# Kernel tuning notes

Hardware: AMD Instinct MI355X
Metric: run time of the kernel (lower is better)

The kernel has to match this reference:

```python
import jax, jax.numpy as jnp
import numpy as np

EPS = 1e-5


def setup_inputs() -> dict:
    key = jax.random.key(0)
    ks = jax.random.split(key, 7)
    B, T, H = 4, 4096, 1024
    x = jax.random.normal(ks[0], (B, T, H), dtype=jnp.float32)
    gamma = jnp.ones((H,), dtype=jnp.float32)
    beta = jnp.zeros((H,), dtype=jnp.float32)
    s = 1.0 / np.sqrt(H)
    Wg = jax.random.uniform(ks[1], (H, H), minval=-s, maxval=s, dtype=jnp.float32)
    bg = jax.random.uniform(ks[2], (H,), minval=-s, maxval=s, dtype=jnp.float32)
    Wc = jax.random.uniform(ks[3], (H, H), minval=-s, maxval=s, dtype=jnp.float32)
    bc = jax.random.uniform(ks[4], (H,), minval=-s, maxval=s, dtype=jnp.float32)
    return {"x": x, "gamma": gamma, "beta": beta, "Wg": Wg, "bg": bg, "Wc": Wc, "bc": bc}


def reference(x, gamma, beta, Wg, bg, Wc, bc):
    # x: [B, T, H]
    mu = jnp.mean(x, axis=-1, keepdims=True)
    var = jnp.mean((x - mu) ** 2, axis=-1, keepdims=True)
    normed = (x - mu) * jax.lax.rsqrt(var + EPS) * gamma + beta
    z = jax.nn.sigmoid(jnp.einsum('bth,oh->bto', normed, Wg) + bg)  # gate
    c = jnp.einsum('bth,oh->bto', normed, Wc) + bc                  # candidate
    B, T, H = x.shape

    def step(h, zc):
        z_t, c_t = zc  # each [B, H]
        h = (1.0 - z_t) * h + z_t * c_t
        return h, h

    h0 = jnp.zeros((B, H), dtype=x.dtype)
    # scan over time: move T to leading axis
    _, hs = jax.lax.scan(step, h0, (jnp.swapaxes(z, 0, 1), jnp.swapaxes(c, 0, 1)))
    return jnp.swapaxes(hs, 0, 1) + x  # residual
```

## Files before the change

kernel.cpp:

```cpp
#include <hip/hip_runtime.h>
#include <stdint.h>


#define B_    4
#define T_    4096
#define H_    1024
#define BT_   (B_*T_)
#define EPSV  1e-5f
#define CHK   32
#define CL    (T_/CHK)

typedef float  f32x4  __attribute__((ext_vector_type(4)));
typedef __bf16 bf16x8 __attribute__((ext_vector_type(8)));
typedef unsigned short u16;

__device__ __forceinline__ u16 f2bf(float f) {
  uint32_t u = __builtin_bit_cast(uint32_t, f);
  u += 0x7fffu + ((u >> 16) & 1u);
  return (u16)(u >> 16);
}
__device__ __forceinline__ float bf2f(u16 u) {
  uint32_t v = ((uint32_t)u) << 16;
  return __builtin_bit_cast(float, v);
}

__global__ __launch_bounds__(256) void ln_kernel(
    const float* __restrict__ x, const float* __restrict__ gamma,
    const float* __restrict__ beta, u16* __restrict__ normed) {
  const int row = blockIdx.x;
  const int tid = threadIdx.x;
  const float4 v = reinterpret_cast<const float4*>(x + (size_t)row * H_)[tid];
  float s = v.x + v.y + v.z + v.w;
  float q = v.x*v.x + v.y*v.y + v.z*v.z + v.w*v.w;
  #pragma unroll
  for (int off = 32; off > 0; off >>= 1) {
    s += __shfl_down(s, off);
    q += __shfl_down(q, off);
  }
  __shared__ float ls[8], lq[8];
  const int wid = tid >> 6, lane = tid & 63;
  if (lane == 0) { ls[wid] = s; lq[wid] = q; }
  __syncthreads();
  if (tid == 0) {
    ls[4] = ls[0] + ls[1] + ls[2] + ls[3];
    lq[4] = lq[0] + lq[1] + lq[2] + lq[3];
  }
  __syncthreads();
  const float mean = ls[4] * (1.0f / H_);
  const float var  = lq[4] * (1.0f / H_) - mean * mean;
  const float rstd = rsqrtf(var + EPSV);
  const float4 g  = reinterpret_cast<const float4*>(gamma)[tid];
  const float4 bb = reinterpret_cast<const float4*>(beta)[tid];
  uint2 o;
  o.x = (uint32_t)f2bf((v.x - mean) * rstd * g.x + bb.x)
      | ((uint32_t)f2bf((v.y - mean) * rstd * g.y + bb.y) << 16);
  o.y = (uint32_t)f2bf((v.z - mean) * rstd * g.z + bb.z)
      | ((uint32_t)f2bf((v.w - mean) * rstd * g.w + bb.w) << 16);
  reinterpret_cast<uint2*>(normed + (size_t)row * H_)[tid] = o;
}

__global__ __launch_bounds__(256) void pack_kernel(
    const float* __restrict__ Wg, const float* __restrict__ Wc,
    u16* __restrict__ wpack) {
  const int idx4 = (blockIdx.x * 256 + threadIdx.x) * 4;
  const int n = idx4 >> 10;
  const int k = idx4 & 1023;
  const float* src = (n < 1024) ? (Wg + (size_t)n * 1024 + k)
                                : (Wc + (size_t)(n - 1024) * 1024 + k);
  const float4 v = *reinterpret_cast<const float4*>(src);
  uint2 o;
  o.x = (uint32_t)f2bf(v.x) | ((uint32_t)f2bf(v.y) << 16);
  o.y = (uint32_t)f2bf(v.z) | ((uint32_t)f2bf(v.w) << 16);
  *reinterpret_cast<uint2*>(wpack + idx4) = o;
}

__global__ __launch_bounds__(256) void gemm_kernel(
    const u16* __restrict__ A, const u16* __restrict__ Bw,
    const float* __restrict__ bg, const float* __restrict__ bc,
    u16* __restrict__ zbuf, u16* __restrict__ cbuf) {
  __shared__ u16 As[128 * 32];
  __shared__ u16 Bs[128 * 32];
  const int bid = blockIdx.x;
  const int nb  = (bid & 7) * 256 + (bid >> 3);
  const int mt  = nb >> 4, nt = nb & 15;
  const int tid = threadIdx.x;
  const int wid = tid >> 6, lane = tid & 63;
  const int wr = wid >> 1, wcq = wid & 1;

  f32x4 acc[4][4] = {};

  const int c0 = tid, c1 = tid + 256;
  const u16* a0 = A  + (size_t)(mt * 128 + (c0 >> 2)) * 1024 + (c0 & 3) * 8;
  const u16* a1 = A  + (size_t)(mt * 128 + (c1 >> 2)) * 1024 + (c1 & 3) * 8;
  const u16* b0 = Bw + (size_t)(nt * 128 + (c0 >> 2)) * 1024 + (c0 & 3) * 8;
  const u16* b1 = Bw + (size_t)(nt * 128 + (c1 >> 2)) * 1024 + (c1 & 3) * 8;

  const int frow = lane & 15;
  const int kb   = (lane >> 4) * 8;

  for (int ks = 0; ks < 32; ++ks) {
    const int kk = ks * 32;
    __builtin_amdgcn_global_load_lds(
        (const __attribute__((address_space(1))) void*)(a0 + kk),
        (__attribute__((address_space(3))) void*)&As[c0 * 8], 16, 0, 0);
    __builtin_amdgcn_global_load_lds(
        (const __attribute__((address_space(1))) void*)(a1 + kk),
        (__attribute__((address_space(3))) void*)&As[c1 * 8], 16, 0, 0);
    __builtin_amdgcn_global_load_lds(
        (const __attribute__((address_space(1))) void*)(b0 + kk),
        (__attribute__((address_space(3))) void*)&Bs[c0 * 8], 16, 0, 0);
    __builtin_amdgcn_global_load_lds(
        (const __attribute__((address_space(1))) void*)(b1 + kk),
        (__attribute__((address_space(3))) void*)&Bs[c1 * 8], 16, 0, 0);
    __syncthreads();

    bf16x8 af[4], bfr[4];
    #pragma unroll
    for (int m = 0; m < 4; ++m)
      af[m] = *reinterpret_cast<const bf16x8*>(&As[(wr * 64 + m * 16 + frow) * 32 + kb]);
    #pragma unroll
    for (int n = 0; n < 4; ++n)
      bfr[n] = *reinterpret_cast<const bf16x8*>(&Bs[(wcq * 64 + n * 16 + frow) * 32 + kb]);
    #pragma unroll
    for (int m = 0; m < 4; ++m)
      #pragma unroll
      for (int n = 0; n < 4; ++n)
        acc[m][n] = __builtin_amdgcn_mfma_f32_16x16x32_bf16(af[m], bfr[n], acc[m][n], 0, 0, 0);
    __syncthreads();
  }

  const int r0  = (lane >> 4) * 4;
  const int col16 = lane & 15;
  const bool isz = (nt < 8);
  #pragma unroll
  for (int m = 0; m < 4; ++m) {
    #pragma unroll
    for (int n = 0; n < 4; ++n) {
      const int col = nt * 128 + wcq * 64 + n * 16 + col16;
      #pragma unroll
      for (int r = 0; r < 4; ++r) {
        const int row = mt * 128 + wr * 64 + m * 16 + r0 + r;
        float v = acc[m][n][r];
        if (isz) {
          v += bg[col];
          v = 1.0f / (1.0f + __expf(-v));
          zbuf[(size_t)row * 1024 + col] = f2bf(v);
        } else {
          const int cc = col - 1024;
          v += bc[cc];
          cbuf[(size_t)row * 1024 + cc] = f2bf(v);
        }
      }
    }
  }
}

__global__ __launch_bounds__(256) void scan1_kernel(
    const u16* __restrict__ zbuf, const u16* __restrict__ cbuf,
    float* __restrict__ Achk, float* __restrict__ Uchk) {
  const int bid   = blockIdx.x;
  const int o     = (bid & 3) * 256 + threadIdx.x;
  const int chunk = (bid >> 2) & 31;
  const int b     = bid >> 7;
  const size_t base = ((size_t)(b * T_ + chunk * CL)) * H_ + o;
  float A = 1.0f, u = 0.0f;
  #pragma unroll 8
  for (int t = 0; t < CL; ++t) {
    const float z = bf2f(zbuf[base + (size_t)t * H_]);
    const float c = bf2f(cbuf[base + (size_t)t * H_]);
    const float a = 1.0f - z;
    A *= a;
    u = a * u + z * c;
  }
  const int idx = (b * CHK + chunk) * H_ + o;
  Achk[idx] = A;
  Uchk[idx] = u;
}

__global__ __launch_bounds__(256) void scan2_kernel(
    const float* __restrict__ Achk, const float* __restrict__ Uchk,
    float* __restrict__ Hin) {
  const int bid = blockIdx.x;
  const int o   = (bid & 3) * 256 + threadIdx.x;
  const int b   = bid >> 2;
  float h = 0.0f;
  for (int j = 0; j < CHK; ++j) {
    const int idx = (b * CHK + j) * H_ + o;
    Hin[idx] = h;
    h = Achk[idx] * h + Uchk[idx];
  }
}

__global__ __launch_bounds__(256) void scan3_kernel(
    const u16* __restrict__ zbuf, const u16* __restrict__ cbuf,
    const float* __restrict__ Hin, const float* __restrict__ x,
    float* __restrict__ out) {
  const int bid   = blockIdx.x;
  const int o     = (bid & 3) * 256 + threadIdx.x;
  const int chunk = (bid >> 2) & 31;
  const int b     = bid >> 7;
  float h = Hin[(b * CHK + chunk) * H_ + o];
  const size_t base = ((size_t)(b * T_ + chunk * CL)) * H_ + o;
  #pragma unroll 4
  for (int t = 0; t < CL; ++t) {
    const size_t idx = base + (size_t)t * H_;
    const float z = bf2f(zbuf[idx]);
    const float c = bf2f(cbuf[idx]);
    h = (1.0f - z) * h + z * c;
    out[idx] = h + x[idx];
  }
}

extern "C" void kernel_launch(void* const* d_in, const int* in_sizes, int n_in,
                              void* d_out, int out_size, void* d_ws, size_t ws_size,
                              hipStream_t stream) {
  const float* x     = (const float*)d_in[0];
  const float* gamma = (const float*)d_in[1];
  const float* beta  = (const float*)d_in[2];
  const float* Wg    = (const float*)d_in[3];
  const float* bg    = (const float*)d_in[4];
  const float* Wc    = (const float*)d_in[5];
  const float* bc    = (const float*)d_in[6];
  float* out = (float*)d_out;

  char* ws = (char*)d_ws;
  u16*   normed = (u16*)(ws);
  u16*   wpack  = (u16*)(ws + 33554432ull);
  u16*   zbuf   = (u16*)(ws + 37748736ull);
  u16*   cbuf   = (u16*)(ws + 71303168ull);
  float* Achk   = (float*)(ws + 104857600ull);
  float* Uchk   = (float*)(ws + 105381888ull);
  float* Hin    = (float*)(ws + 105906176ull);

  ln_kernel  <<<BT_,  256, 0, stream>>>(x, gamma, beta, normed);
  pack_kernel<<<2048, 256, 0, stream>>>(Wg, Wc, wpack);
  gemm_kernel<<<2048, 256, 0, stream>>>(normed, wpack, bg, bc, zbuf, cbuf);
  scan1_kernel<<<512, 256, 0, stream>>>(zbuf, cbuf, Achk, Uchk);
  scan2_kernel<<<16,  256, 0, stream>>>(Achk, Uchk, Hin);
  scan3_kernel<<<512, 256, 0, stream>>>(zbuf, cbuf, Hin, x, out);
}
```

Baseline: 287.0 us.

## Double-buffer GEMM LDS, vectorize scans, warp-per-row layernorm, finer scan chunks

Several changes land together. The GEMM now double-buffers its LDS tiles so the next K-slice is fetched while the current one is computed. LayerNorm handles one row per wavefront with xor shuffles, which removes the shared-memory reduction and both barriers. The scan kernels move to 128 chunks with each thread handling four columns through vectorized bf16 and float loads, and the chunk-state buffers now reuse the normed region of the workspace. The gain in parallelism and load width is paid for with more LDS per GEMM block and a longer serial pass in scan2.

```diff
diff --git a/kernel.cpp b/kernel.cpp
--- a/kernel.cpp
+++ b/kernel.cpp
@@ -7,7 +7,7 @@
 #define H_    1024
 #define BT_   (B_*T_)
 #define EPSV  1e-5f
-#define CHK   32
+#define CHK   128
 #define CL    (T_/CHK)
 
 typedef float  f32x4  __attribute__((ext_vector_type(4)));
@@ -19,44 +19,51 @@
   u += 0x7fffu + ((u >> 16) & 1u);
   return (u16)(u >> 16);
 }
-__device__ __forceinline__ float bf2f(u16 u) {
-  uint32_t v = ((uint32_t)u) << 16;
+__device__ __forceinline__ float bf2f(uint32_t u) {
+  uint32_t v = (u & 0xffffu) << 16;
   return __builtin_bit_cast(float, v);
+}
+__device__ __forceinline__ void bf4(uint2 p, float* f) {
+  f[0] = bf2f(p.x); f[1] = bf2f(p.x >> 16);
+  f[2] = bf2f(p.y); f[3] = bf2f(p.y >> 16);
 }
 
 __global__ __launch_bounds__(256) void ln_kernel(
     const float* __restrict__ x, const float* __restrict__ gamma,
     const float* __restrict__ beta, u16* __restrict__ normed) {
-  const int row = blockIdx.x;
-  const int tid = threadIdx.x;
-  const float4 v = reinterpret_cast<const float4*>(x + (size_t)row * H_)[tid];
-  float s = v.x + v.y + v.z + v.w;
-  float q = v.x*v.x + v.y*v.y + v.z*v.z + v.w*v.w;
-  #pragma unroll
-  for (int off = 32; off > 0; off >>= 1) {
-    s += __shfl_down(s, off);
-    q += __shfl_down(q, off);
-  }
-  __shared__ float ls[8], lq[8];
-  const int wid = tid >> 6, lane = tid & 63;
-  if (lane == 0) { ls[wid] = s; lq[wid] = q; }
-  __syncthreads();
-  if (tid == 0) {
-    ls[4] = ls[0] + ls[1] + ls[2] + ls[3];
-    lq[4] = lq[0] + lq[1] + lq[2] + lq[3];
-  }
-  __syncthreads();
-  const float mean = ls[4] * (1.0f / H_);
-  const float var  = lq[4] * (1.0f / H_) - mean * mean;
+  const int wid  = threadIdx.x >> 6, lane = threadIdx.x & 63;
+  const int row  = blockIdx.x * 4 + wid;
+  const float4* xr = reinterpret_cast<const float4*>(x + (size_t)row * H_);
+  float4 v[4];
+  float s = 0.0f, q = 0.0f;
+  #pragma unroll
+  for (int seg = 0; seg < 4; ++seg) {
+    v[seg] = xr[seg * 64 + lane];
+    s += v[seg].x + v[seg].y + v[seg].z + v[seg].w;
+    q += v[seg].x*v[seg].x + v[seg].y*v[seg].y + v[seg].z*v[seg].z + v[seg].w*v[seg].w;
+  }
+  #pragma unroll
+  for (int off = 1; off < 64; off <<= 1) {
+    s += __shfl_xor(s, off);
+    q += __shfl_xor(q, off);
+  }
+  const float mean = s * (1.0f / H_);
+  const float var  = q * (1.0f / H_) - mean * mean;
   const float rstd = rsqrtf(var + EPSV);
-  const float4 g  = reinterpret_cast<const float4*>(gamma)[tid];
-  const float4 bb = reinterpret_cast<const float4*>(beta)[tid];
-  uint2 o;
-  o.x = (uint32_t)f2bf((v.x - mean) * rstd * g.x + bb.x)
-      | ((uint32_t)f2bf((v.y - mean) * rstd * g.y + bb.y) << 16);
-  o.y = (uint32_t)f2bf((v.z - mean) * rstd * g.z + bb.z)
-      | ((uint32_t)f2bf((v.w - mean) * rstd * g.w + bb.w) << 16);
-  reinterpret_cast<uint2*>(normed + (size_t)row * H_)[tid] = o;
+  const float4* g4 = reinterpret_cast<const float4*>(gamma);
+  const float4* b4 = reinterpret_cast<const float4*>(beta);
+  uint2* o2 = reinterpret_cast<uint2*>(normed + (size_t)row * H_);
+  #pragma unroll
+  for (int seg = 0; seg < 4; ++seg) {
+    const float4 g = g4[seg * 64 + lane];
+    const float4 b = b4[seg * 64 + lane];
+    uint2 o;
+    o.x = (uint32_t)f2bf((v[seg].x - mean) * rstd * g.x + b.x)
+        | ((uint32_t)f2bf((v[seg].y - mean) * rstd * g.y + b.y) << 16);
+    o.y = (uint32_t)f2bf((v[seg].z - mean) * rstd * g.z + b.z)
+        | ((uint32_t)f2bf((v[seg].w - mean) * rstd * g.w + b.w) << 16);
+    o2[seg * 64 + lane] = o;
+  }
 }
 
 __global__ __launch_bounds__(256) void pack_kernel(
@@ -78,8 +85,8 @@
     const u16* __restrict__ A, const u16* __restrict__ Bw,
     const float* __restrict__ bg, const float* __restrict__ bc,
     u16* __restrict__ zbuf, u16* __restrict__ cbuf) {
-  __shared__ u16 As[128 * 32];
-  __shared__ u16 Bs[128 * 32];
+  __shared__ u16 As[2][128 * 32];
+  __shared__ u16 Bs[2][128 * 32];
   const int bid = blockIdx.x;
   const int nb  = (bid & 7) * 256 + (bid >> 3);
   const int mt  = nb >> 4, nt = nb & 15;
@@ -98,36 +105,46 @@
   const int frow = lane & 15;
   const int kb   = (lane >> 4) * 8;
 
-  for (int ks = 0; ks < 32; ++ks) {
+  auto stage = [&](int buf, int ks) {
     const int kk = ks * 32;
     __builtin_amdgcn_global_load_lds(
         (const __attribute__((address_space(1))) void*)(a0 + kk),
-        (__attribute__((address_space(3))) void*)&As[c0 * 8], 16, 0, 0);
+        (__attribute__((address_space(3))) void*)&As[buf][c0 * 8], 16, 0, 0);
     __builtin_amdgcn_global_load_lds(
         (const __attribute__((address_space(1))) void*)(a1 + kk),
-        (__attribute__((address_space(3))) void*)&As[c1 * 8], 16, 0, 0);
+        (__attribute__((address_space(3))) void*)&As[buf][c1 * 8], 16, 0, 0);
     __builtin_amdgcn_global_load_lds(
         (const __attribute__((address_space(1))) void*)(b0 + kk),
-        (__attribute__((address_space(3))) void*)&Bs[c0 * 8], 16, 0, 0);
+        (__attribute__((address_space(3))) void*)&Bs[buf][c0 * 8], 16, 0, 0);
     __builtin_amdgcn_global_load_lds(
         (const __attribute__((address_space(1))) void*)(b1 + kk),
-        (__attribute__((address_space(3))) void*)&Bs[c1 * 8], 16, 0, 0);
-    __syncthreads();
-
+        (__attribute__((address_space(3))) void*)&Bs[buf][c1 * 8], 16, 0, 0);
+  };
+  auto compute = [&](int buf) {
     bf16x8 af[4], bfr[4];
     #pragma unroll
     for (int m = 0; m < 4; ++m)
-      af[m] = *reinterpret_cast<const bf16x8*>(&As[(wr * 64 + m * 16 + frow) * 32 + kb]);
+      af[m] = *reinterpret_cast<const bf16x8*>(&As[buf][(wr * 64 + m * 16 + frow) * 32 + kb]);
     #pragma unroll
     for (int n = 0; n < 4; ++n)
-      bfr[n] = *reinterpret_cast<const bf16x8*>(&Bs[(wcq * 64 + n * 16 + frow) * 32 + kb]);
+      bfr[n] = *reinterpret_cast<const bf16x8*>(&Bs[buf][(wcq * 64 + n * 16 + frow) * 32 + kb]);
     #pragma unroll
     for (int m = 0; m < 4; ++m)
       #pragma unroll
       for (int n = 0; n < 4; ++n)
         acc[m][n] = __builtin_amdgcn_mfma_f32_16x16x32_bf16(af[m], bfr[n], acc[m][n], 0, 0, 0);
+  };
+
+  stage(0, 0);
+  __syncthreads();
+  int cur = 0;
+  for (int ks = 0; ks < 31; ++ks) {
+    stage(cur ^ 1, ks + 1);
+    compute(cur);
     __syncthreads();
-  }
+    cur ^= 1;
+  }
+  compute(cur);
 
   const int r0  = (lane >> 4) * 4;
   const int col16 = lane & 15;
@@ -159,31 +176,39 @@
     const u16* __restrict__ zbuf, const u16* __restrict__ cbuf,
     float* __restrict__ Achk, float* __restrict__ Uchk) {
   const int bid   = blockIdx.x;
-  const int o     = (bid & 3) * 256 + threadIdx.x;
-  const int chunk = (bid >> 2) & 31;
+  const int chunk = bid & (CHK - 1);
   const int b     = bid >> 7;
-  const size_t base = ((size_t)(b * T_ + chunk * CL)) * H_ + o;
-  float A = 1.0f, u = 0.0f;
-  #pragma unroll 8
+  const int o4    = threadIdx.x * 4;
+  const size_t base = ((size_t)(b * T_ + chunk * CL)) * H_ + o4;
+  float A[4] = {1.f, 1.f, 1.f, 1.f};
+  float u[4] = {0.f, 0.f, 0.f, 0.f};
+  #pragma unroll 4
   for (int t = 0; t < CL; ++t) {
-    const float z = bf2f(zbuf[base + (size_t)t * H_]);
-    const float c = bf2f(cbuf[base + (size_t)t * H_]);
-    const float a = 1.0f - z;
-    A *= a;
-    u = a * u + z * c;
-  }
-  const int idx = (b * CHK + chunk) * H_ + o;
-  Achk[idx] = A;
-  Uchk[idx] = u;
+    const size_t idx = base + (size_t)t * H_;
+    const uint2 zp = *reinterpret_cast<const uint2*>(&zbuf[idx]);
+    const uint2 cp = *reinterpret_cast<const uint2*>(&cbuf[idx]);
+    float z[4], c[4];
+    bf4(zp, z); bf4(cp, c);
+    #pragma unroll
+    for (int j = 0; j < 4; ++j) {
+      const float a = 1.0f - z[j];
+      A[j] *= a;
+      u[j] = a * u[j] + z[j] * c[j];
+    }
+  }
+  const int idx = (b * CHK + chunk) * H_ + o4;
+  *reinterpret_cast<float4*>(&Achk[idx]) = make_float4(A[0], A[1], A[2], A[3]);
+  *reinterpret_cast<float4*>(&Uchk[idx]) = make_float4(u[0], u[1], u[2], u[3]);
 }
 
 __global__ __launch_bounds__(256) void scan2_kernel(
     const float* __restrict__ Achk, const float* __restrict__ Uchk,
     float* __restrict__ Hin) {
-  const int bid = blockIdx.x;
-  const int o   = (bid & 3) * 256 + threadIdx.x;
-  const int b   = bid >> 2;
+  const int g = blockIdx.x * 256 + threadIdx.x;
+  const int b = g >> 10;
+  const int o = g & 1023;
   float h = 0.0f;
+  #pragma unroll 8
   for (int j = 0; j < CHK; ++j) {
     const int idx = (b * CHK + j) * H_ + o;
     Hin[idx] = h;
@@ -196,18 +221,25 @@
     const float* __restrict__ Hin, const float* __restrict__ x,
     float* __restrict__ out) {
   const int bid   = blockIdx.x;
-  const int o     = (bid & 3) * 256 + threadIdx.x;
-  const int chunk = (bid >> 2) & 31;
+  const int chunk = bid & (CHK - 1);
   const int b     = bid >> 7;
-  float h = Hin[(b * CHK + chunk) * H_ + o];
-  const size_t base = ((size_t)(b * T_ + chunk * CL)) * H_ + o;
+  const int o4    = threadIdx.x * 4;
+  const float4 hv = *reinterpret_cast<const float4*>(&Hin[(b * CHK + chunk) * H_ + o4]);
+  float h[4] = {hv.x, hv.y, hv.z, hv.w};
+  const size_t base = ((size_t)(b * T_ + chunk * CL)) * H_ + o4;
   #pragma unroll 4
   for (int t = 0; t < CL; ++t) {
     const size_t idx = base + (size_t)t * H_;
-    const float z = bf2f(zbuf[idx]);
-    const float c = bf2f(cbuf[idx]);
-    h = (1.0f - z) * h + z * c;
-    out[idx] = h + x[idx];
+    const uint2 zp = *reinterpret_cast<const uint2*>(&zbuf[idx]);
+    const uint2 cp = *reinterpret_cast<const uint2*>(&cbuf[idx]);
+    const float4 xv = *reinterpret_cast<const float4*>(&x[idx]);
+    float z[4], c[4];
+    bf4(zp, z); bf4(cp, c);
+    #pragma unroll
+    for (int j = 0; j < 4; ++j)
+      h[j] = (1.0f - z[j]) * h[j] + z[j] * c[j];
+    *reinterpret_cast<float4*>(&out[idx]) =
+        make_float4(h[0] + xv.x, h[1] + xv.y, h[2] + xv.z, h[3] + xv.w);
   }
 }
 
@@ -228,14 +260,14 @@
   u16*   wpack  = (u16*)(ws + 33554432ull);
   u16*   zbuf   = (u16*)(ws + 37748736ull);
   u16*   cbuf   = (u16*)(ws + 71303168ull);
-  float* Achk   = (float*)(ws + 104857600ull);
-  float* Uchk   = (float*)(ws + 105381888ull);
-  float* Hin    = (float*)(ws + 105906176ull);
-
-  ln_kernel  <<<BT_,  256, 0, stream>>>(x, gamma, beta, normed);
-  pack_kernel<<<2048, 256, 0, stream>>>(Wg, Wc, wpack);
-  gemm_kernel<<<2048, 256, 0, stream>>>(normed, wpack, bg, bc, zbuf, cbuf);
-  scan1_kernel<<<512, 256, 0, stream>>>(zbuf, cbuf, Achk, Uchk);
-  scan2_kernel<<<16,  256, 0, stream>>>(Achk, Uchk, Hin);
-  scan3_kernel<<<512, 256, 0, stream>>>(zbuf, cbuf, Hin, x, out);
-}
+  float* Achk   = (float*)(ws);
+  float* Uchk   = (float*)(ws + 2097152ull);
+  float* Hin    = (float*)(ws + 4194304ull);
+
+  ln_kernel  <<<BT_/4, 256, 0, stream>>>(x, gamma, beta, normed);
+  pack_kernel<<<2048,  256, 0, stream>>>(Wg, Wc, wpack);
+  gemm_kernel<<<2048,  256, 0, stream>>>(normed, wpack, bg, bc, zbuf, cbuf);
+  scan1_kernel<<<B_*CHK, 256, 0, stream>>>(zbuf, cbuf, Achk, Uchk);
+  scan2_kernel<<<16,     256, 0, stream>>>(Achk, Uchk, Hin);
+  scan3_kernel<<<B_*CHK, 256, 0, stream>>>(zbuf, cbuf, Hin, x, out);
+}
```

Measured after the change: 298.3 us. 1.04x slower.
